# Optimization experiments

Hardware: AMD Instinct MI355X
Metric: run time of the kernel (lower is better)

Reference implementation:

```python
import jax, jax.numpy as jnp
import numpy as np

N_NODES = 30000
N_EDGES = 480000
IN_FEATS = 256
H_FEATS = 128
HEADS = 4
OUT_DIM = 128
NEG_SLOPE = 0.2  # PyG GATConv default leaky_relu slope


def gat_conv(x, src, dst, W, att_src, att_dst, bias, concat):
    """PyG-style GATConv (eval mode, self-loops already in src/dst).
    x: [N, Fin]; W: [Fin, H*C]; att_src/att_dst: [H, C]; bias: [H*C] or [C].
    """
    N = x.shape[0]
    H, C = att_src.shape
    h = (x @ W).reshape(N, H, C)                       # [N, H, C]
    a_src = jnp.einsum('nhc,hc->nh', h, att_src)       # [N, H]
    a_dst = jnp.einsum('nhc,hc->nh', h, att_dst)
    e = jax.nn.leaky_relu(a_src[src] + a_dst[dst], NEG_SLOPE)  # [E, H]
    # segment softmax over incoming edges of each dst node
    m = jax.ops.segment_max(e, dst, num_segments=N)    # [N, H]
    m = jnp.where(jnp.isfinite(m), m, 0.0)
    ex = jnp.exp(e - m[dst])
    denom = jax.ops.segment_sum(ex, dst, num_segments=N)
    alpha = ex / denom[dst]                            # [E, H]
    msg = alpha[:, :, None] * h[src]                   # [E, H, C]
    out = jax.ops.segment_sum(msg, dst, num_segments=N)  # [N, H, C]
    if concat:
        out = out.reshape(N, H * C)
    else:
        out = out.mean(axis=1)
    return out + bias


def setup_inputs() -> dict:
    key = jax.random.key(0)
    ks = jax.random.split(key, 12)
    s = 0.05
    x = jax.random.normal(ks[0], (N_NODES, IN_FEATS), dtype=jnp.float32)
    edge_index = jax.random.randint(ks[1], (2, N_EDGES), 0, N_NODES, dtype=jnp.int64)
    W1 = jax.random.normal(ks[2], (IN_FEATS, HEADS * H_FEATS), dtype=jnp.float32) * s
    att_src1 = jax.random.normal(ks[3], (HEADS, H_FEATS), dtype=jnp.float32) * s
    att_dst1 = jax.random.normal(ks[4], (HEADS, H_FEATS), dtype=jnp.float32) * s
    b1 = jnp.zeros((HEADS * H_FEATS,), dtype=jnp.float32)
    W2 = jax.random.normal(ks[5], (HEADS * H_FEATS, HEADS * H_FEATS), dtype=jnp.float32) * s
    att_src2 = jax.random.normal(ks[6], (HEADS, H_FEATS), dtype=jnp.float32) * s
    att_dst2 = jax.random.normal(ks[7], (HEADS, H_FEATS), dtype=jnp.float32) * s
    b2 = jnp.zeros((HEADS * H_FEATS,), dtype=jnp.float32)
    W3 = jax.random.normal(ks[8], (HEADS * H_FEATS, OUT_DIM), dtype=jnp.float32) * s
    att_src3 = jax.random.normal(ks[9], (1, OUT_DIM), dtype=jnp.float32) * s
    att_dst3 = jax.random.normal(ks[10], (1, OUT_DIM), dtype=jnp.float32) * s
    b3 = jnp.zeros((OUT_DIM,), dtype=jnp.float32)
    return {"x": x, "edge_index": edge_index,
            "W1": W1, "att_src1": att_src1, "att_dst1": att_dst1, "b1": b1,
            "W2": W2, "att_src2": att_src2, "att_dst2": att_dst2, "b2": b2,
            "W3": W3, "att_src3": att_src3, "att_dst3": att_dst3, "b3": b3}


def reference(x, edge_index, W1, att_src1, att_dst1, b1,
              W2, att_src2, att_dst2, b2, W3, att_src3, att_dst3, b3):
    # PyG GATConv adds self-loops by default
    loops = jnp.arange(N_NODES, dtype=edge_index.dtype)
    src = jnp.concatenate([edge_index[0], loops])
    dst = jnp.concatenate([edge_index[1], loops])
    h = gat_conv(x, src, dst, W1, att_src1, att_dst1, b1, concat=True)
    h = jax.nn.relu(h)  # dropout inactive in eval mode
    h = gat_conv(h, src, dst, W2, att_src2, att_dst2, b2, concat=True)
    h = jax.nn.relu(h)
    out = gat_conv(h, src, dst, W3, att_src3, att_dst3, b3, concat=False)
    return out
```

## Files before the change

### kernel.cpp

```cpp
#include <hip/hip_runtime.h>


#define NEG_SLOPE 0.2f

typedef __attribute__((ext_vector_type(8))) short short8;
typedef __attribute__((ext_vector_type(4))) float floatx4;

static __device__ __forceinline__ unsigned short f2bf(float f) {
    unsigned u = __float_as_uint(f);
    u = u + 0x7FFFu + ((u >> 16) & 1u);
    return (unsigned short)(u >> 16);
}
static __device__ __forceinline__ float bf2f_lo(unsigned u) {
    return __uint_as_float(u << 16);
}
static __device__ __forceinline__ float bf2f_hi(unsigned u) {
    return __uint_as_float(u & 0xFFFF0000u);
}

static __device__ __forceinline__ void async_copy16(const void* g, void* l) {
    __builtin_amdgcn_global_load_lds(
        (const __attribute__((address_space(1))) unsigned int*)g,
        (__attribute__((address_space(3))) unsigned int*)l, 16, 0, 0);
}


__global__ __launch_bounds__(256)
void prep_kernel(const float* __restrict__ x, unsigned short* __restrict__ x_bf,
                 const float* __restrict__ W1, unsigned short* __restrict__ W1T,
                 const float* __restrict__ W2, unsigned short* __restrict__ W2T,
                 const float* __restrict__ W3, unsigned short* __restrict__ W3T,
                 int n4) {
    int i = blockIdx.x * 256 + threadIdx.x;
    if (i < n4) {
        float4 v = ((const float4*)x)[i];
        ushort4 o;
        o.x = f2bf(v.x); o.y = f2bf(v.y); o.z = f2bf(v.z); o.w = f2bf(v.w);
        ((ushort4*)x_bf)[i] = o;
        return;
    }
    int j = i - n4;
    if (j < 256 * 512) {
        int k = j >> 9, n = j & 511;
        W1T[(size_t)n * 256 + k] = f2bf(W1[j]);
    } else if ((j -= 256 * 512) < 512 * 512) {
        int k = j >> 9, n = j & 511;
        W2T[(size_t)n * 512 + k] = f2bf(W2[j]);
    } else if ((j -= 512 * 512) < 512 * 128) {
        int k = j >> 7, n = j & 127;
        W3T[(size_t)n * 512 + k] = f2bf(W3[j]);
    }
}


__global__ __launch_bounds__(256)
void hist_kernel(const int* __restrict__ ei, int* cursor, int E) {
    int e = blockIdx.x * 256 + threadIdx.x;
    if (e < E) atomicAdd(&cursor[ei[E + e]], 1);
}

__global__ __launch_bounds__(1024)
void scan_bsum_kernel(const int* __restrict__ cursor, int* __restrict__ bsum, int N) {
    __shared__ int wsum[16];
    int tid = threadIdx.x, lane = tid & 63, w = tid >> 6;
    int i = blockIdx.x * 1024 + tid;
    int v = (i < N) ? cursor[i] : 0;
    #pragma unroll
    for (int off = 32; off; off >>= 1) v += __shfl_xor(v, off, 64);
    if (lane == 0) wsum[w] = v;
    __syncthreads();
    if (tid == 0) {
        int t = 0;
        #pragma unroll
        for (int k = 0; k < 16; ++k) t += wsum[k];
        bsum[blockIdx.x] = t;
    }
}

__global__ __launch_bounds__(64)
void scan_boffs_kernel(const int* __restrict__ bsum, int* __restrict__ boffs,
                       int NB, int* __restrict__ row_ptr, int N) {
    int lane = threadIdx.x;
    int v = (lane < NB) ? bsum[lane] : 0;
    int x = v;
    #pragma unroll
    for (int off = 1; off < 64; off <<= 1) {
        int t = __shfl_up(x, off, 64);
        if (lane >= off) x += t;
    }
    if (lane < NB) boffs[lane] = x - v;
    if (lane == 63) row_ptr[N] = x + N;
}

__global__ __launch_bounds__(1024)
void scan_final_kernel(int* __restrict__ cursor, const int* __restrict__ boffs,
                       int* __restrict__ row_ptr, int N) {
    __shared__ int wsum[16];
    int tid = threadIdx.x, lane = tid & 63, w = tid >> 6;
    int i = blockIdx.x * 1024 + tid;
    int v = (i < N) ? cursor[i] : 0;
    int x = v;
    #pragma unroll
    for (int off = 1; off < 64; off <<= 1) {
        int t = __shfl_up(x, off, 64);
        if (lane >= off) x += t;
    }
    if (lane == 63) wsum[w] = x;
    __syncthreads();
    if (w == 0 && lane < 16) {
        int y = wsum[lane];
        #pragma unroll
        for (int off = 1; off < 16; off <<= 1) {
            int t = __shfl_up(y, off, 64);
            if (lane >= off) y += t;
        }
        wsum[lane] = y;
    }
    __syncthreads();
    int woff = (w == 0) ? 0 : wsum[w - 1];
    int ex = boffs[blockIdx.x] + woff + x - v + i;
    if (i < N) { row_ptr[i] = ex; cursor[i] = ex; }
}

__global__ __launch_bounds__(256)
void scatter_kernel(const int* __restrict__ ei, int* cursor,
                    int* __restrict__ csr_src, int E, int N) {
    int i = blockIdx.x * 256 + threadIdx.x;
    if (i < E) {
        int s = ei[i], d = ei[E + i];
        int pos = atomicAdd(&cursor[d], 1);
        csr_src[pos] = s;
    } else if (i < E + N) {
        int n = i - E;
        int pos = atomicAdd(&cursor[n], 1);
        csr_src[pos] = n;
    }
}


__global__ __launch_bounds__(256)
void mfma_gemm_kernel(const unsigned short* __restrict__ A,
                      const unsigned short* __restrict__ BT,
                      unsigned short* __restrict__ C,
                      const float* __restrict__ att_src,
                      const float* __restrict__ att_dst,
                      float* __restrict__ a_srcO, float* __restrict__ a_dstO,
                      int H, int M, int Nn, int K) {
    __shared__ unsigned short As[128 * 32];
    __shared__ unsigned short Bs[128 * 32];
    __shared__ float psum[2][128];
    __shared__ float pdsum[2][128];
    const int tid = threadIdx.x;
    const int m0 = blockIdx.y * 128;
    const int n0 = blockIdx.x * 128;
    const int head = blockIdx.x;
    const int lane = tid & 63, wave = tid >> 6;
    const int wm = (wave & 1) * 64, wn = (wave >> 1) * 64;
    const int quad = lane >> 4, rr = lane & 15;

    const int r16 = lane >> 2;
    const int phys = lane & 3;
    const int rowL0 = wave * 32 + r16;
    const int rowL1 = wave * 32 + 16 + r16;
    const int seg0 = phys ^ ((rowL0 >> 1) & 3);
    const int seg1 = phys ^ ((rowL1 >> 1) & 3);
    const int gmA0 = min(m0 + rowL0, M - 1);
    const int gmA1 = min(m0 + rowL1, M - 1);
    const int gnB0 = n0 + rowL0;
    const int gnB1 = n0 + rowL1;
    unsigned short* ldsA0 = As + (wave * 32) * 32;
    unsigned short* ldsA1 = As + (wave * 32 + 16) * 32;
    unsigned short* ldsB0 = Bs + (wave * 32) * 32;
    unsigned short* ldsB1 = Bs + (wave * 32 + 16) * 32;

    const int swz = quad ^ ((rr >> 1) & 3);

    floatx4 acc[4][4] = {};

    for (int k0 = 0; k0 < K; k0 += 32) {
        async_copy16(A  + (size_t)gmA0 * K + k0 + seg0 * 8, ldsA0);
        async_copy16(A  + (size_t)gmA1 * K + k0 + seg1 * 8, ldsA1);
        async_copy16(BT + (size_t)gnB0 * K + k0 + seg0 * 8, ldsB0);
        async_copy16(BT + (size_t)gnB1 * K + k0 + seg1 * 8, ldsB1);
        __syncthreads();

        short8 af[4], bf[4];
        #pragma unroll
        for (int mi = 0; mi < 4; ++mi)
            af[mi] = *(const short8*)(As + (wm + mi * 16 + rr) * 32 + swz * 8);
        #pragma unroll
        for (int ni = 0; ni < 4; ++ni)
            bf[ni] = *(const short8*)(Bs + (wn + ni * 16 + rr) * 32 + swz * 8);
        #pragma unroll
        for (int mi = 0; mi < 4; ++mi)
            #pragma unroll
            for (int ni = 0; ni < 4; ++ni)
                acc[mi][ni] = __builtin_amdgcn_mfma_f32_16x16x32_bf16(
                    af[mi], bf[ni], acc[mi][ni], 0, 0, 0);
        __syncthreads();
    }

    #pragma unroll
    for (int mi = 0; mi < 4; ++mi) {
        #pragma unroll
        for (int ni = 0; ni < 4; ++ni) {
            int col = n0 + wn + ni * 16 + rr;
            #pragma unroll
            for (int r = 0; r < 4; ++r) {
                int row = m0 + wm + mi * 16 + quad * 4 + r;
                if (row < M) C[(size_t)row * Nn + col] = f2bf(acc[mi][ni][r]);
            }
        }
    }

    float ats[4], atd[4];
    #pragma unroll
    for (int ni = 0; ni < 4; ++ni) {
        int c = wn + ni * 16 + rr;
        ats[ni] = att_src[head * 128 + c];
        atd[ni] = att_dst[head * 128 + c];
    }
    const int wnh = wn >> 6;
    #pragma unroll
    for (int mi = 0; mi < 4; ++mi) {
        #pragma unroll
        for (int r = 0; r < 4; ++r) {
            float ps = 0.f, pd = 0.f;
            #pragma unroll
            for (int ni = 0; ni < 4; ++ni) {
                ps += ats[ni] * acc[mi][ni][r];
                pd += atd[ni] * acc[mi][ni][r];
            }
            #pragma unroll
            for (int off = 1; off < 16; off <<= 1) {
                ps += __shfl_xor(ps, off, 64);
                pd += __shfl_xor(pd, off, 64);
            }
            if (rr == 0) {
                int row = wm + mi * 16 + quad * 4 + r;
                psum[wnh][row] = ps;
                pdsum[wnh][row] = pd;
            }
        }
    }
    __syncthreads();
    if (tid < 128) {
        int gr = m0 + tid;
        if (gr < M) {
            a_srcO[(size_t)gr * H + head] = psum[0][tid] + psum[1][tid];
            a_dstO[(size_t)gr * H + head] = pdsum[0][tid] + pdsum[1][tid];
        }
    }
}


template<int F, int H, bool RELU, bool BF16OUT>
__global__ __launch_bounds__(256)
void agg_kernel(const unsigned* __restrict__ hfeat, const float* __restrict__ a_src,
                const float* __restrict__ a_dst, const int* __restrict__ row_ptr,
                const int* __restrict__ csr_src, const float* __restrict__ bias,
                void* __restrict__ out_v, int N) {
    constexpr int UPL = F / 128;
    constexpr int RU = F / 2;
    const int wave = threadIdx.x >> 6, lane = threadIdx.x & 63;
    const int n = blockIdx.x * 4 + wave;
    if (n >= N) return;
    const int begin = __builtin_amdgcn_readfirstlane(row_ptr[n]);
    const int deg = __builtin_amdgcn_readfirstlane(row_ptr[n + 1]) - begin;
    const int myh = (2 * UPL * lane) / 128;
    const float adst = a_dst[n * H + myh];

    float acc[2 * UPL];
    #pragma unroll
    for (int j = 0; j < 2 * UPL; ++j) acc[j] = 0.f;
    float dacc = 0.f;

    unsigned u0[UPL], u1[UPL], u2[UPL], u3[UPL];
    float av0 = 0.f, av1 = 0.f, av2 = 0.f, av3 = 0.f;

#define LOADSLOT(idx, U, AV)                                              \
    {                                                                     \
        int s_ = __builtin_amdgcn_readfirstlane(csr_src[begin + (idx)]);  \
        if (UPL == 4) {                                                   \
            uint4 t_ = ((const uint4*)(hfeat + (size_t)s_ * RU))[lane];   \
            U[0] = t_.x; U[1] = t_.y; U[2] = t_.z; U[3] = t_.w;           \
        } else {                                                          \
            U[0] = hfeat[(size_t)s_ * RU + lane];                         \
        }                                                                 \
        AV = a_src[s_ * H + myh];                                         \
    }

#define CONSUME(U, AV)                                                    \
    {                                                                     \
        float e_ = AV + adst;                                             \
        e_ = e_ > 0.f ? e_ : NEG_SLOPE * e_;                              \
        float ex_ = __expf(e_);                                           \
        dacc += ex_;                                                      \
        _Pragma("unroll")                                                 \
        for (int q_ = 0; q_ < UPL; ++q_) {                                \
            acc[2 * q_]     += ex_ * bf2f_lo(U[q_]);                      \
            acc[2 * q_ + 1] += ex_ * bf2f_hi(U[q_]);                      \
        }                                                                 \
    }

    LOADSLOT(0, u0, av0);
    if (deg > 1) LOADSLOT(1, u1, av1);
    if (deg > 2) LOADSLOT(2, u2, av2);
    if (deg > 3) LOADSLOT(3, u3, av3);
    int i = 0;
    for (; i + 8 <= deg; i += 4) {
        CONSUME(u0, av0); LOADSLOT(i + 4, u0, av0);
        CONSUME(u1, av1); LOADSLOT(i + 5, u1, av1);
        CONSUME(u2, av2); LOADSLOT(i + 6, u2, av2);
        CONSUME(u3, av3); LOADSLOT(i + 7, u3, av3);
    }
    int rem = deg - i;
    CONSUME(u0, av0); if (rem > 4) LOADSLOT(i + 4, u0, av0);
    if (rem > 1) { CONSUME(u1, av1); if (rem > 5) LOADSLOT(i + 5, u1, av1); }
    if (rem > 2) { CONSUME(u2, av2); if (rem > 6) LOADSLOT(i + 6, u2, av2); }
    if (rem > 3) CONSUME(u3, av3);
    if (rem > 4) CONSUME(u0, av0);
    if (rem > 5) CONSUME(u1, av1);
    if (rem > 6) CONSUME(u2, av2);
#undef LOADSLOT
#undef CONSUME

    float inv = 1.f / dacc;
    const int cb = 2 * UPL * lane;
    if (BF16OUT) {
        unsigned pk[UPL];
        #pragma unroll
        for (int q = 0; q < UPL; ++q) {
            float v0 = acc[2 * q] * inv + bias[cb + 2 * q];
            float v1 = acc[2 * q + 1] * inv + bias[cb + 2 * q + 1];
            if (RELU) { v0 = fmaxf(v0, 0.f); v1 = fmaxf(v1, 0.f); }
            pk[q] = (unsigned)f2bf(v0) | ((unsigned)f2bf(v1) << 16);
        }
        if (UPL == 4) {
            uint4 t; t.x = pk[0]; t.y = pk[1]; t.z = pk[2]; t.w = pk[3];
            ((uint4*)((unsigned*)out_v + (size_t)n * RU))[lane] = t;
        } else {
            ((unsigned*)out_v)[(size_t)n * RU + lane] = pk[0];
        }
    } else {
        #pragma unroll
        for (int q = 0; q < UPL; ++q) {
            float v0 = acc[2 * q] * inv + bias[cb + 2 * q];
            float v1 = acc[2 * q + 1] * inv + bias[cb + 2 * q + 1];
            if (RELU) { v0 = fmaxf(v0, 0.f); v1 = fmaxf(v1, 0.f); }
            float2 o; o.x = v0; o.y = v1;
            ((float2*)((float*)out_v + (size_t)n * F))[UPL * lane + q] = o;
        }
    }
}


extern "C" void kernel_launch(void* const* d_in, const int* in_sizes, int n_in,
                              void* d_out, int out_size, void* d_ws, size_t ws_size,
                              hipStream_t stream) {
    const float* x        = (const float*)d_in[0];
    const int*   ei       = (const int*)  d_in[1];
    const float* W1       = (const float*)d_in[2];
    const float* att_src1 = (const float*)d_in[3];
    const float* att_dst1 = (const float*)d_in[4];
    const float* b1       = (const float*)d_in[5];
    const float* W2       = (const float*)d_in[6];
    const float* att_src2 = (const float*)d_in[7];
    const float* att_dst2 = (const float*)d_in[8];
    const float* b2       = (const float*)d_in[9];
    const float* W3       = (const float*)d_in[10];
    const float* att_src3 = (const float*)d_in[11];
    const float* att_dst3 = (const float*)d_in[12];
    const float* b3       = (const float*)d_in[13];

    const int IN_FEATS = 256;
    const int N = in_sizes[0] / IN_FEATS;
    const int E = in_sizes[1] / 2;
    const int ET = E + N;
    const int NB = (N + 1023) / 1024;

    char* p = (char*)d_ws;
    unsigned short* h_bf    = (unsigned short*)p; p += (size_t)N * 512 * sizeof(unsigned short);
    unsigned short* act_bf  = (unsigned short*)p; p += (size_t)N * 512 * sizeof(unsigned short);
    unsigned short* x_bf    = (unsigned short*)p; p += (size_t)N * 256 * sizeof(unsigned short);
    float*          a_src   = (float*)p;          p += (size_t)N * 4 * sizeof(float);
    float*          a_dst   = (float*)p;          p += (size_t)N * 4 * sizeof(float);
    unsigned short* W1T     = (unsigned short*)p; p += (size_t)512 * 256 * sizeof(unsigned short);
    unsigned short* W2T     = (unsigned short*)p; p += (size_t)512 * 512 * sizeof(unsigned short);
    unsigned short* W3T     = (unsigned short*)p; p += (size_t)128 * 512 * sizeof(unsigned short);
    int*            row_ptr = (int*)p;            p += ((size_t)N + 16) * sizeof(int);
    int*            cursor  = (int*)p;            p += ((size_t)N + 16) * sizeof(int);
    int*            bsum    = (int*)p;            p += 64 * sizeof(int);
    int*            boffs   = (int*)p;            p += 64 * sizeof(int);
    int*            csr_src = (int*)p;            p += (size_t)ET * sizeof(int);

    hipMemsetAsync(cursor, 0, (size_t)N * sizeof(int), stream);
    {
        int n4 = N * 256 / 4;
        int total = n4 + 256 * 512 + 512 * 512 + 512 * 128;
        prep_kernel<<<(total + 255) / 256, 256, 0, stream>>>(
            x, x_bf, W1, W1T, W2, W2T, W3, W3T, n4);
    }
    hist_kernel<<<(E + 255) / 256, 256, 0, stream>>>(ei, cursor, E);
    scan_bsum_kernel<<<NB, 1024, 0, stream>>>(cursor, bsum, N);
    scan_boffs_kernel<<<1, 64, 0, stream>>>(bsum, boffs, NB, row_ptr, N);
    scan_final_kernel<<<NB, 1024, 0, stream>>>(cursor, boffs, row_ptr, N);
    scatter_kernel<<<(E + N + 255) / 256, 256, 0, stream>>>(ei, cursor, csr_src, E, N);

    const int MB = (N + 127) / 128;
    const int NB4 = (N + 3) / 4;

    mfma_gemm_kernel<<<dim3(4, MB), 256, 0, stream>>>(x_bf, W1T, h_bf, att_src1, att_dst1, a_src, a_dst, 4, N, 512, 256);
    agg_kernel<512, 4, true, true><<<NB4, 256, 0, stream>>>((const unsigned*)h_bf, a_src, a_dst, row_ptr, csr_src, b1, act_bf, N);

    mfma_gemm_kernel<<<dim3(4, MB), 256, 0, stream>>>(act_bf, W2T, h_bf, att_src2, att_dst2, a_src, a_dst, 4, N, 512, 512);
    agg_kernel<512, 4, true, true><<<NB4, 256, 0, stream>>>((const unsigned*)h_bf, a_src, a_dst, row_ptr, csr_src, b2, act_bf, N);

    mfma_gemm_kernel<<<dim3(1, MB), 256, 0, stream>>>(act_bf, W3T, h_bf, att_src3, att_dst3, a_src, a_dst, 1, N, 128, 512);
    agg_kernel<128, 1, false, false><<<NB4, 256, 0, stream>>>((const unsigned*)h_bf, a_src, a_dst, row_ptr, csr_src, b3, d_out, N);
}
```

Baseline: 415.8 us.

## Fuse prep with histogram, merge scan kernels, deepen GEMM K-tile to 64

Folds the edge histogram into the prep kernel and removes the separate block-offset scan kernel by recomputing the 64-entry prefix in each final-scan block, which cuts two launches. Separately, the MFMA GEMM now stages a 64-wide K slice per iteration with a new XOR swizzle, halving the number of barrier pairs and doing two MFMA sub-steps per load. This doubles LDS use per block, which may lower occupancy.

```diff
diff --git a/kernel.cpp b/kernel.cpp
--- a/kernel.cpp
+++ b/kernel.cpp
@@ -26,11 +26,11 @@
 
 
 __global__ __launch_bounds__(256)
-void prep_kernel(const float* __restrict__ x, unsigned short* __restrict__ x_bf,
-                 const float* __restrict__ W1, unsigned short* __restrict__ W1T,
-                 const float* __restrict__ W2, unsigned short* __restrict__ W2T,
-                 const float* __restrict__ W3, unsigned short* __restrict__ W3T,
-                 int n4) {
+void prep_hist_kernel(const float* __restrict__ x, unsigned short* __restrict__ x_bf,
+                      const float* __restrict__ W1, unsigned short* __restrict__ W1T,
+                      const float* __restrict__ W2, unsigned short* __restrict__ W2T,
+                      const float* __restrict__ W3, unsigned short* __restrict__ W3T,
+                      const int* __restrict__ ei, int* cursor, int n4, int E) {
     int i = blockIdx.x * 256 + threadIdx.x;
     if (i < n4) {
         float4 v = ((const float4*)x)[i];
@@ -43,21 +43,24 @@
     if (j < 256 * 512) {
         int k = j >> 9, n = j & 511;
         W1T[(size_t)n * 256 + k] = f2bf(W1[j]);
-    } else if ((j -= 256 * 512) < 512 * 512) {
+        return;
+    }
+    j -= 256 * 512;
+    if (j < 512 * 512) {
         int k = j >> 9, n = j & 511;
         W2T[(size_t)n * 512 + k] = f2bf(W2[j]);
-    } else if ((j -= 512 * 512) < 512 * 128) {
+        return;
+    }
+    j -= 512 * 512;
+    if (j < 512 * 128) {
         int k = j >> 7, n = j & 127;
         W3T[(size_t)n * 512 + k] = f2bf(W3[j]);
-    }
-}
-
-
-__global__ __launch_bounds__(256)
-void hist_kernel(const int* __restrict__ ei, int* cursor, int E) {
-    int e = blockIdx.x * 256 + threadIdx.x;
-    if (e < E) atomicAdd(&cursor[ei[E + e]], 1);
-}
+        return;
+    }
+    j -= 512 * 128;
+    if (j < E) atomicAdd(&cursor[ei[E + j]], 1);
+}
+
 
 __global__ __launch_bounds__(1024)
 void scan_bsum_kernel(const int* __restrict__ cursor, int* __restrict__ bsum, int N) {
@@ -77,26 +80,23 @@
     }
 }
 
-__global__ __launch_bounds__(64)
-void scan_boffs_kernel(const int* __restrict__ bsum, int* __restrict__ boffs,
-                       int NB, int* __restrict__ row_ptr, int N) {
-    int lane = threadIdx.x;
-    int v = (lane < NB) ? bsum[lane] : 0;
-    int x = v;
-    #pragma unroll
-    for (int off = 1; off < 64; off <<= 1) {
-        int t = __shfl_up(x, off, 64);
-        if (lane >= off) x += t;
-    }
-    if (lane < NB) boffs[lane] = x - v;
-    if (lane == 63) row_ptr[N] = x + N;
-}
-
 __global__ __launch_bounds__(1024)
-void scan_final_kernel(int* __restrict__ cursor, const int* __restrict__ boffs,
-                       int* __restrict__ row_ptr, int N) {
+void scan_final_kernel(int* __restrict__ cursor, const int* __restrict__ bsum,
+                       int* __restrict__ row_ptr, int N, int NB) {
     __shared__ int wsum[16];
+    __shared__ int boff_sh;
     int tid = threadIdx.x, lane = tid & 63, w = tid >> 6;
+    if (w == 0) {
+        int bv = (lane < NB) ? bsum[lane] : 0;
+        int bx = bv;
+        #pragma unroll
+        for (int off = 1; off < 64; off <<= 1) {
+            int t = __shfl_up(bx, off, 64);
+            if (lane >= off) bx += t;
+        }
+        if (lane == blockIdx.x) boff_sh = bx - bv;
+        if (blockIdx.x == 0 && lane == 63) row_ptr[N] = bx + N;
+    }
     int i = blockIdx.x * 1024 + tid;
     int v = (i < N) ? cursor[i] : 0;
     int x = v;
@@ -118,7 +118,7 @@
     }
     __syncthreads();
     int woff = (w == 0) ? 0 : wsum[w - 1];
-    int ex = boffs[blockIdx.x] + woff + x - v + i;
+    int ex = boff_sh + woff + x - v + i;
     if (i < N) { row_ptr[i] = ex; cursor[i] = ex; }
 }
 
@@ -146,8 +146,8 @@
                       const float* __restrict__ att_dst,
                       float* __restrict__ a_srcO, float* __restrict__ a_dstO,
                       int H, int M, int Nn, int K) {
-    __shared__ unsigned short As[128 * 32];
-    __shared__ unsigned short Bs[128 * 32];
+    __shared__ unsigned short As[128 * 64];
+    __shared__ unsigned short Bs[128 * 64];
     __shared__ float psum[2][128];
     __shared__ float pdsum[2][128];
     const int tid = threadIdx.x;
@@ -158,45 +158,50 @@
     const int wm = (wave & 1) * 64, wn = (wave >> 1) * 64;
     const int quad = lane >> 4, rr = lane & 15;
 
-    const int r16 = lane >> 2;
-    const int phys = lane & 3;
-    const int rowL0 = wave * 32 + r16;
-    const int rowL1 = wave * 32 + 16 + r16;
-    const int seg0 = phys ^ ((rowL0 >> 1) & 3);
-    const int seg1 = phys ^ ((rowL1 >> 1) & 3);
-    const int gmA0 = min(m0 + rowL0, M - 1);
-    const int gmA1 = min(m0 + rowL1, M - 1);
-    const int gnB0 = n0 + rowL0;
-    const int gnB1 = n0 + rowL1;
-    unsigned short* ldsA0 = As + (wave * 32) * 32;
-    unsigned short* ldsA1 = As + (wave * 32 + 16) * 32;
-    unsigned short* ldsB0 = Bs + (wave * 32) * 32;
-    unsigned short* ldsB1 = Bs + (wave * 32 + 16) * 32;
-
-    const int swz = quad ^ ((rr >> 1) & 3);
+    const int srow = lane >> 3;
+    const int sseg = (lane & 7) ^ srow;
+    int gArow[4], gBrow[4];
+    #pragma unroll
+    for (int j = 0; j < 4; ++j) {
+        int rowL = wave * 32 + j * 8 + srow;
+        gArow[j] = min(m0 + rowL, M - 1);
+        gBrow[j] = n0 + rowL;
+    }
 
     floatx4 acc[4][4] = {};
 
-    for (int k0 = 0; k0 < K; k0 += 32) {
-        async_copy16(A  + (size_t)gmA0 * K + k0 + seg0 * 8, ldsA0);
-        async_copy16(A  + (size_t)gmA1 * K + k0 + seg1 * 8, ldsA1);
-        async_copy16(BT + (size_t)gnB0 * K + k0 + seg0 * 8, ldsB0);
-        async_copy16(BT + (size_t)gnB1 * K + k0 + seg1 * 8, ldsB1);
+    for (int k0 = 0; k0 < K; k0 += 64) {
+        #pragma unroll
+        for (int j = 0; j < 4; ++j) {
+            async_copy16(A  + (size_t)gArow[j] * K + k0 + sseg * 8,
+                         As + (wave * 32 + j * 8) * 64);
+            async_copy16(BT + (size_t)gBrow[j] * K + k0 + sseg * 8,
+                         Bs + (wave * 32 + j * 8) * 64);
+        }
         __syncthreads();
 
-        short8 af[4], bf[4];
-        #pragma unroll
-        for (int mi = 0; mi < 4; ++mi)
-            af[mi] = *(const short8*)(As + (wm + mi * 16 + rr) * 32 + swz * 8);
-        #pragma unroll
-        for (int ni = 0; ni < 4; ++ni)
-            bf[ni] = *(const short8*)(Bs + (wn + ni * 16 + rr) * 32 + swz * 8);
-        #pragma unroll
-        for (int mi = 0; mi < 4; ++mi)
-            #pragma unroll
-            for (int ni = 0; ni < 4; ++ni)
-                acc[mi][ni] = __builtin_amdgcn_mfma_f32_16x16x32_bf16(
-                    af[mi], bf[ni], acc[mi][ni], 0, 0, 0);
+        #pragma unroll
+        for (int k32 = 0; k32 < 2; ++k32) {
+            short8 af[4], bf[4];
+            #pragma unroll
+            for (int mi = 0; mi < 4; ++mi) {
+                int row = wm + mi * 16 + rr;
+                int phys = (k32 * 4 + quad) ^ (rr & 7);
+                af[mi] = *(const short8*)(As + row * 64 + phys * 8);
+            }
+            #pragma unroll
+            for (int ni = 0; ni < 4; ++ni) {
+                int row = wn + ni * 16 + rr;
+                int phys = (k32 * 4 + quad) ^ (rr & 7);
+                bf[ni] = *(const short8*)(Bs + row * 64 + phys * 8);
+            }
+            #pragma unroll
+            for (int mi = 0; mi < 4; ++mi)
+                #pragma unroll
+                for (int ni = 0; ni < 4; ++ni)
+                    acc[mi][ni] = __builtin_amdgcn_mfma_f32_16x16x32_bf16(
+                        af[mi], bf[ni], acc[mi][ni], 0, 0, 0);
+        }
         __syncthreads();
     }
 
@@ -391,20 +396,17 @@
     int*            row_ptr = (int*)p;            p += ((size_t)N + 16) * sizeof(int);
     int*            cursor  = (int*)p;            p += ((size_t)N + 16) * sizeof(int);
     int*            bsum    = (int*)p;            p += 64 * sizeof(int);
-    int*            boffs   = (int*)p;            p += 64 * sizeof(int);
     int*            csr_src = (int*)p;            p += (size_t)ET * sizeof(int);
 
     hipMemsetAsync(cursor, 0, (size_t)N * sizeof(int), stream);
     {
         int n4 = N * 256 / 4;
-        int total = n4 + 256 * 512 + 512 * 512 + 512 * 128;
-        prep_kernel<<<(total + 255) / 256, 256, 0, stream>>>(
-            x, x_bf, W1, W1T, W2, W2T, W3, W3T, n4);
-    }
-    hist_kernel<<<(E + 255) / 256, 256, 0, stream>>>(ei, cursor, E);
+        int total = n4 + 256 * 512 + 512 * 512 + 512 * 128 + E;
+        prep_hist_kernel<<<(total + 255) / 256, 256, 0, stream>>>(
+            x, x_bf, W1, W1T, W2, W2T, W3, W3T, ei, cursor, n4, E);
+    }
     scan_bsum_kernel<<<NB, 1024, 0, stream>>>(cursor, bsum, N);
-    scan_boffs_kernel<<<1, 64, 0, stream>>>(bsum, boffs, NB, row_ptr, N);
-    scan_final_kernel<<<NB, 1024, 0, stream>>>(cursor, boffs, row_ptr, N);
+    scan_final_kernel<<<NB, 1024, 0, stream>>>(cursor, bsum, row_ptr, N, NB);
     scatter_kernel<<<(E + N + 255) / 256, 256, 0, stream>>>(ei, cursor, csr_src, E, N);
 
     const int MB = (N + 127) / 128;
```

Result: no change. 408.8 us (-1.7%).
